# Kernel tuning notes

Measured on AMD Instinct MI355X. Metric: run time of the kernel, lower is better.

Reference implementation:

```python
import jax, jax.numpy as jnp
import numpy as np
import math

D_MODEL = 1024
N_HEADS = 16
D_HEAD = D_MODEL // N_HEADS


def setup_inputs() -> dict:
    key = jax.random.key(0)
    ks = jax.random.split(key, 5)
    scale = 1.0 / math.sqrt(D_MODEL)
    x = jax.random.normal(ks[0], (4, 2048, D_MODEL), dtype=jnp.float32)
    W_q = jax.random.uniform(ks[1], (D_MODEL, D_MODEL), jnp.float32, -scale, scale)
    W_k = jax.random.uniform(ks[2], (D_MODEL, D_MODEL), jnp.float32, -scale, scale)
    W_v = jax.random.uniform(ks[3], (D_MODEL, D_MODEL), jnp.float32, -scale, scale)
    W_o = jax.random.uniform(ks[4], (D_MODEL, D_MODEL), jnp.float32, -scale, scale)
    return {"x": x, "W_q": W_q, "W_k": W_k, "W_v": W_v, "W_o": W_o}


def reference(x, W_q, W_k, W_v, W_o):
    B, S, D = x.shape
    H, Dh = N_HEADS, D_HEAD
    # nn.Linear(bias=False): y = x @ W.T
    q = (x @ W_q.T).reshape(B, S, H, Dh).transpose(0, 2, 1, 3)  # [B,H,S,Dh]
    k = (x @ W_k.T).reshape(B, S, H, Dh).transpose(0, 2, 1, 3)
    v = (x @ W_v.T).reshape(B, S, H, Dh).transpose(0, 2, 1, 3)
    scores = jnp.einsum('bhqd,bhkd->bhqk', q, k) / math.sqrt(Dh)  # [B,H,S,S]
    causal = jnp.triu(jnp.ones((S, S), dtype=bool), k=1)
    scores = jnp.where(causal, jnp.float32(-1e9), scores)
    attn = jax.nn.softmax(scores, axis=-1)  # dropout = identity (eval)
    out = jnp.einsum('bhqk,bhkd->bhqd', attn, v)  # [B,H,S,Dh]
    out = out.transpose(0, 2, 1, 3).reshape(B, S, D)
    return out @ W_o.T
```

## Files before the change

kernel.cpp:

```cpp
#include <hip/hip_runtime.h>
#include <hip/hip_bf16.h>

typedef __attribute__((ext_vector_type(8))) short short8;
typedef __attribute__((ext_vector_type(4))) float f32x4;
typedef __attribute__((ext_vector_type(16))) float f32x16;
typedef __attribute__((ext_vector_type(4))) unsigned short u16x4;

#define S_LEN 2048
#define DH 64
#define NH 16
#define SCALE_LOG2 0.18033688011112042f
#define EXP2F(x) __builtin_amdgcn_exp2f(x)
#define GLOAD_LDS16(src, dst)                                             \
  __builtin_amdgcn_global_load_lds(                                       \
      (const __attribute__((address_space(1))) void*)(src),               \
      (__attribute__((address_space(3))) void*)(dst), 16, 0, 0)

__device__ __forceinline__ unsigned short f2bf(float f) {
  unsigned int u = __float_as_uint(f);
  u += 0x7fffu + ((u >> 16) & 1u);
  return (unsigned short)(u >> 16);
}

__device__ __forceinline__ unsigned int cvtpk(float a, float b) {
  unsigned int r;
  asm("v_cvt_pk_bf16_f32 %0, %1, %2" : "=v"(r) : "v"(a), "v"(b));
  return r;
}
__device__ __forceinline__ void plswap(unsigned int& a, unsigned int& b) {
  asm("v_permlane32_swap_b32 %0, %1" : "+v"(a), "+v"(b));
}

__global__ void convert_all(const float* __restrict__ x,
                            const float* __restrict__ w0,
                            const float* __restrict__ w1,
                            const float* __restrict__ w2,
                            const float* __restrict__ w3,
                            unsigned short* __restrict__ xb,
                            unsigned short* __restrict__ o0,
                            unsigned short* __restrict__ o1,
                            unsigned short* __restrict__ o2,
                            unsigned short* __restrict__ o3) {
  const int bid = blockIdx.x;
  const float* in;
  unsigned short* out;
  int i;
  if (bid < 8192) {
    in = x; out = xb;
    i = (bid * 256 + threadIdx.x) * 4;
  } else {
    const int seg = (bid - 8192) >> 10;
    in  = (seg == 0) ? w0 : (seg == 1) ? w1 : (seg == 2) ? w2 : w3;
    out = (seg == 0) ? o0 : (seg == 1) ? o1 : (seg == 2) ? o2 : o3;
    i = (((bid - 8192) & 1023) * 256 + threadIdx.x) * 4;
  }
  float4 v = *reinterpret_cast<const float4*>(in + i);
  u16x4 o;
  o.x = f2bf(v.x); o.y = f2bf(v.y); o.z = f2bf(v.z); o.w = f2bf(v.w);
  *reinterpret_cast<u16x4*>(out + i) = o;
}

template <int MODE>
__global__ __launch_bounds__(256) void gemm_bt(
    const unsigned short* __restrict__ A,
    const unsigned short* __restrict__ B,
    void* __restrict__ out, int M, int N, int K) {
  __shared__ __align__(16) unsigned short As[128 * 64];
  __shared__ __align__(16) unsigned short Bs[128 * 64];
  const int tid = threadIdx.x;
  const int l = tid & 63, w = tid >> 6;
  const int wr = w >> 1, wc = w & 1;
  const int g = l >> 4, c = l & 15;
  const int m0 = blockIdx.y * 128;
  const int n0 = blockIdx.x * 128;
  const int lrow = l >> 3, lcol = (l & 7) * 8;

  f32x4 acc[4][4] = {};

  for (int k0 = 0; k0 < K; k0 += 64) {
#pragma unroll
    for (int p = 0; p < 4; ++p) {
      int r0 = w * 32 + p * 8;
      GLOAD_LDS16(&A[(long)(m0 + r0 + lrow) * K + k0 + lcol], &As[r0 * 64]);
      GLOAD_LDS16(&B[(long)(n0 + r0 + lrow) * K + k0 + lcol], &Bs[r0 * 64]);
    }
    __syncthreads();
#pragma unroll
    for (int s = 0; s < 2; ++s) {
      short8 af[4], bf[4];
#pragma unroll
      for (int m = 0; m < 4; ++m)
        af[m] = *reinterpret_cast<const short8*>(
            &As[(wr * 64 + m * 16 + c) * 64 + s * 32 + g * 8]);
#pragma unroll
      for (int n = 0; n < 4; ++n)
        bf[n] = *reinterpret_cast<const short8*>(
            &Bs[(wc * 64 + n * 16 + c) * 64 + s * 32 + g * 8]);
#pragma unroll
      for (int m = 0; m < 4; ++m)
#pragma unroll
        for (int n = 0; n < 4; ++n)
          acc[m][n] = __builtin_amdgcn_mfma_f32_16x16x32_bf16(
              af[m], bf[n], acc[m][n], 0, 0, 0);
    }
    __syncthreads();
  }

#pragma unroll
  for (int m = 0; m < 4; ++m) {
#pragma unroll
    for (int n = 0; n < 4; ++n) {
#pragma unroll
      for (int r = 0; r < 4; ++r) {
        int row = m0 + wr * 64 + m * 16 + g * 4 + r;
        int col = n0 + wc * 64 + n * 16 + c;
        float v = acc[m][n][r];
        if (MODE == 3) {
          reinterpret_cast<float*>(out)[(long)row * N + col] = v;
        } else if (MODE == 2) {
          int b = row >> 11, s = row & 2047;
          int h = col >> 6, d = col & 63;
          reinterpret_cast<unsigned short*>(
              out)[((long)((b * NH + h) * DH + d)) * S_LEN + s] = f2bf(v);
        } else {
          if (MODE == 1) v *= SCALE_LOG2;
          int b = row >> 11, s = row & 2047;
          int h = col >> 6, d = col & 63;
          reinterpret_cast<unsigned short*>(
              out)[((long)((b * NH + h) * S_LEN + s)) * DH + d] = f2bf(v);
        }
      }
    }
  }
}

__device__ __forceinline__ int swz8c(int row, int chunk) {
  return row * 64 + ((chunk ^ (row & 7)) << 3);
}

__global__ __launch_bounds__(256) void attn_fwd(
    const unsigned short* __restrict__ Q, const unsigned short* __restrict__ Kg,
    const unsigned short* __restrict__ Vt, unsigned short* __restrict__ O) {
  __shared__ __align__(16) unsigned short Ks[2][64 * 64];
  __shared__ __align__(16) unsigned short Vs[2][64 * 64];

  const int tid = threadIdx.x;
  const int l = tid & 63, w = tid >> 6;
  const int ln = l & 31, hi = l >> 5, hi4 = hi * 4;
  const int bh = blockIdx.x;
  const int qb = 15 - blockIdx.y;
  const int b = bh >> 4, h = bh & 15;
  const long base = (long)bh * (S_LEN * DH);
  const int sr8 = l >> 3;
  const int scol = ((l & 7) ^ sr8) * 8;
  const int q0w = qb * 128 + w * 32;

  short8 qf[4];
  {
    const unsigned short* qp = Q + base + (long)(q0w + ln) * DH + hi * 8;
#pragma unroll
    for (int ks = 0; ks < 4; ++ks)
      qf[ks] = *reinterpret_cast<const short8*>(qp + ks * 16);
  }

  f32x16 o0 = {}, o1 = {};
  float m_r = -1e30f, l_r = 0.f;
  const int ntb = qb * 2 + 2;
  const int ntw = q0w / 64 + 1;

#pragma unroll
  for (int p = 0; p < 2; ++p) {
    int r0 = w * 16 + p * 8;
    GLOAD_LDS16(&Kg[base + (long)(r0 + sr8) * DH + scol], &Ks[0][r0 * 64]);
    GLOAD_LDS16(&Vt[base + (long)(r0 + sr8) * S_LEN + scol], &Vs[0][r0 * 64]);
  }
  __syncthreads();

  int cur = 0;
  for (int t = 0; t < ntb; ++t) {
    if (t + 1 < ntb) {
      const int kv1 = (t + 1) * 64;
#pragma unroll
      for (int p = 0; p < 2; ++p) {
        int r0 = w * 16 + p * 8;
        GLOAD_LDS16(&Kg[base + (long)(kv1 + r0 + sr8) * DH + scol],
                    &Ks[cur ^ 1][r0 * 64]);
        GLOAD_LDS16(&Vt[base + (long)(r0 + sr8) * S_LEN + kv1 + scol],
                    &Vs[cur ^ 1][r0 * 64]);
      }
    }
    if (t < ntw) {
      const unsigned short* ksb = Ks[cur];
      const unsigned short* vsb = Vs[cur];
      const int kv0 = t * 64;

      f32x16 s0 = {}, s1 = {};
      __builtin_amdgcn_s_setprio(1);
#pragma unroll
      for (int ks = 0; ks < 4; ++ks) {
        short8 ak0 =
            *reinterpret_cast<const short8*>(&ksb[swz8c(ln, ks * 2 + hi)]);
        short8 ak1 = *reinterpret_cast<const short8*>(
            &ksb[swz8c(32 + ln, ks * 2 + hi)]);
        s0 = __builtin_amdgcn_mfma_f32_32x32x16_bf16(ak0, qf[ks], s0, 0, 0, 0);
        s1 = __builtin_amdgcn_mfma_f32_32x32x16_bf16(ak1, qf[ks], s1, 0, 0, 0);
      }
      __builtin_amdgcn_s_setprio(0);

      if (t == ntw - 1) {
        const int qrel = (q0w - kv0) + ln;
#pragma unroll
        for (int r = 0; r < 16; ++r) {
          const int rowv = (r & 3) + 8 * (r >> 2) + hi4;
          if (rowv > qrel) s0[r] = -1e30f;
          if (rowv + 32 > qrel) s1[r] = -1e30f;
        }
      }

      float pm = -1e30f;
#pragma unroll
      for (int r = 0; r < 16; ++r) pm = fmaxf(pm, fmaxf(s0[r], s1[r]));
      pm = fmaxf(pm, __shfl_xor(pm, 32, 64));

      if (!__all(pm <= m_r + 8.0f)) {
        float mn = fmaxf(m_r, pm);
        float sc = EXP2F(m_r - mn);
        m_r = mn;
        l_r *= sc;
#pragma unroll
        for (int r = 0; r < 16; ++r) {
          float sv = __shfl(sc, (r & 3) + 8 * (r >> 2) + hi4, 64);
          o0[r] *= sv;
          o1[r] *= sv;
        }
      }

      float ps = 0.f;
#pragma unroll
      for (int r = 0; r < 16; ++r) {
        s0[r] = EXP2F(s0[r] - m_r);
        s1[r] = EXP2F(s1[r] - m_r);
        ps += s0[r] + s1[r];
      }
      ps += __shfl_xor(ps, 32, 64);
      l_r += ps;

      __builtin_amdgcn_s_setprio(1);
#pragma unroll
      for (int ks = 0; ks < 4; ++ks) {
        unsigned int wa, wb, wc2, wd;
        if (ks == 0) {
          wa = cvtpk(s0[0], s0[1]);   wc2 = cvtpk(s0[2], s0[3]);
          wb = cvtpk(s0[4], s0[5]);   wd  = cvtpk(s0[6], s0[7]);
        } else if (ks == 1) {
          wa = cvtpk(s0[8], s0[9]);   wc2 = cvtpk(s0[10], s0[11]);
          wb = cvtpk(s0[12], s0[13]); wd  = cvtpk(s0[14], s0[15]);
        } else if (ks == 2) {
          wa = cvtpk(s1[0], s1[1]);   wc2 = cvtpk(s1[2], s1[3]);
          wb = cvtpk(s1[4], s1[5]);   wd  = cvtpk(s1[6], s1[7]);
        } else {
          wa = cvtpk(s1[8], s1[9]);   wc2 = cvtpk(s1[10], s1[11]);
          wb = cvtpk(s1[12], s1[13]); wd  = cvtpk(s1[14], s1[15]);
        }
        plswap(wa, wb);
        plswap(wc2, wd);
        union { unsigned int u[4]; short8 s; } pa;
        pa.u[0] = wa; pa.u[1] = wc2; pa.u[2] = wb; pa.u[3] = wd;
        short8 v0 =
            *reinterpret_cast<const short8*>(&vsb[swz8c(ln, ks * 2 + hi)]);
        short8 v1 = *reinterpret_cast<const short8*>(
            &vsb[swz8c(32 + ln, ks * 2 + hi)]);
        o0 = __builtin_amdgcn_mfma_f32_32x32x16_bf16(pa.s, v0, o0, 0, 0, 0);
        o1 = __builtin_amdgcn_mfma_f32_32x32x16_bf16(pa.s, v1, o1, 0, 0, 0);
      }
      __builtin_amdgcn_s_setprio(0);
    }
    __syncthreads();
    cur ^= 1;
  }

  float inv = 1.0f / l_r;
#pragma unroll
  for (int r = 0; r < 16; ++r) {
    const int rowv = (r & 3) + 8 * (r >> 2) + hi4;
    float iv = __shfl(inv, rowv, 64);
    int q = q0w + rowv;
    long ob = ((long)(b * S_LEN + q)) * 1024 + h * 64 + ln;
    O[ob] = f2bf(o0[r] * iv);
    O[ob + 32] = f2bf(o1[r] * iv);
  }
}

extern "C" void kernel_launch(void* const* d_in, const int* in_sizes, int n_in,
                              void* d_out, int out_size, void* d_ws,
                              size_t ws_size, hipStream_t stream) {
  const float* x  = (const float*)d_in[0];
  const float* Wq = (const float*)d_in[1];
  const float* Wk = (const float*)d_in[2];
  const float* Wv = (const float*)d_in[3];
  const float* Wo = (const float*)d_in[4];
  float* out = (float*)d_out;
  char* ws = (char*)d_ws;

  unsigned short* xb  = (unsigned short*)(ws);
  unsigned short* Wqb = (unsigned short*)(ws + (16u << 20));
  unsigned short* Wkb = (unsigned short*)(ws + (18u << 20));
  unsigned short* Wvb = (unsigned short*)(ws + (20u << 20));
  unsigned short* Wob = (unsigned short*)(ws + (22u << 20));
  unsigned short* Vt  = (unsigned short*)(ws + (24u << 20));
  unsigned short* Ow  = (unsigned short*)(ws);
  unsigned short* Qw = (unsigned short*)d_out;
  unsigned short* Kw = (unsigned short*)d_out + (8u << 20);

  convert_all<<<12288, 256, 0, stream>>>(x, Wq, Wk, Wv, Wo, xb, Wqb, Wkb, Wvb,
                                         Wob);

  dim3 ggrid(8, 64);
  gemm_bt<1><<<ggrid, 256, 0, stream>>>(xb, Wqb, Qw, 8192, 1024, 1024);
  gemm_bt<0><<<ggrid, 256, 0, stream>>>(xb, Wkb, Kw, 8192, 1024, 1024);
  gemm_bt<2><<<ggrid, 256, 0, stream>>>(xb, Wvb, Vt, 8192, 1024, 1024);

  attn_fwd<<<dim3(64, 16), 256, 0, stream>>>(Qw, Kw, Vt, Ow);

  gemm_bt<3><<<ggrid, 256, 0, stream>>>(Ow, Wob, out, 8192, 1024, 1024);
}
```

Before: 194.9 us.

## Merge Q/K/V projection GEMMs into one launch with 8-wave blocks

The three separate Q, K and V projection GEMM launches become one launch, with blockIdx.z picking the weight matrix and the output layout. GEMM blocks grow from 4 to 8 waves, each wave now computing a 32x64 sub-tile instead of 64x64, which halves per-wave accumulator registers and adds waves for latency hiding. The output GEMM uses the same 8-wave configuration. The aim is to cut launch gaps and tail effects and to raise occupancy. The cost is less MFMA work per LDS fragment load for each wave and more intra-block synchronisation pressure.

Result: slower. 203.2 us (+4.3%).

```diff
diff --git a/kernel.cpp b/kernel.cpp
--- a/kernel.cpp
+++ b/kernel.cpp
@@ -61,10 +61,11 @@
 }
 
 template <int MODE>
-__global__ __launch_bounds__(256) void gemm_bt(
+__global__ __launch_bounds__(512) void gemm_bt(
     const unsigned short* __restrict__ A,
     const unsigned short* __restrict__ B,
-    void* __restrict__ out, int M, int N, int K) {
+    void* __restrict__ outQ, void* __restrict__ outK, void* __restrict__ outV,
+    int M, int N, int K) {
   __shared__ __align__(16) unsigned short As[128 * 64];
   __shared__ __align__(16) unsigned short Bs[128 * 64];
   const int tid = threadIdx.x;
@@ -73,31 +74,33 @@
   const int g = l >> 4, c = l & 15;
   const int m0 = blockIdx.y * 128;
   const int n0 = blockIdx.x * 128;
+  const int which = (MODE == 4) ? blockIdx.z : 0;
+  if (MODE == 4) B += (long)which << 20;
   const int lrow = l >> 3, lcol = (l & 7) * 8;
 
-  f32x4 acc[4][4] = {};
+  f32x4 acc[2][4] = {};
 
   for (int k0 = 0; k0 < K; k0 += 64) {
 #pragma unroll
-    for (int p = 0; p < 4; ++p) {
-      int r0 = w * 32 + p * 8;
+    for (int p = 0; p < 2; ++p) {
+      int r0 = p * 64 + w * 8;
       GLOAD_LDS16(&A[(long)(m0 + r0 + lrow) * K + k0 + lcol], &As[r0 * 64]);
       GLOAD_LDS16(&B[(long)(n0 + r0 + lrow) * K + k0 + lcol], &Bs[r0 * 64]);
     }
     __syncthreads();
 #pragma unroll
     for (int s = 0; s < 2; ++s) {
-      short8 af[4], bf[4];
-#pragma unroll
-      for (int m = 0; m < 4; ++m)
+      short8 af[2], bf[4];
+#pragma unroll
+      for (int m = 0; m < 2; ++m)
         af[m] = *reinterpret_cast<const short8*>(
-            &As[(wr * 64 + m * 16 + c) * 64 + s * 32 + g * 8]);
+            &As[(wr * 32 + m * 16 + c) * 64 + s * 32 + g * 8]);
 #pragma unroll
       for (int n = 0; n < 4; ++n)
         bf[n] = *reinterpret_cast<const short8*>(
             &Bs[(wc * 64 + n * 16 + c) * 64 + s * 32 + g * 8]);
 #pragma unroll
-      for (int m = 0; m < 4; ++m)
+      for (int m = 0; m < 2; ++m)
 #pragma unroll
         for (int n = 0; n < 4; ++n)
           acc[m][n] = __builtin_amdgcn_mfma_f32_16x16x32_bf16(
@@ -107,27 +110,30 @@
   }
 
 #pragma unroll
-  for (int m = 0; m < 4; ++m) {
+  for (int m = 0; m < 2; ++m) {
 #pragma unroll
     for (int n = 0; n < 4; ++n) {
 #pragma unroll
       for (int r = 0; r < 4; ++r) {
-        int row = m0 + wr * 64 + m * 16 + g * 4 + r;
+        int row = m0 + wr * 32 + m * 16 + g * 4 + r;
         int col = n0 + wc * 64 + n * 16 + c;
         float v = acc[m][n][r];
         if (MODE == 3) {
-          reinterpret_cast<float*>(out)[(long)row * N + col] = v;
-        } else if (MODE == 2) {
+          reinterpret_cast<float*>(outQ)[(long)row * N + col] = v;
+        } else {
           int b = row >> 11, s = row & 2047;
           int h = col >> 6, d = col & 63;
-          reinterpret_cast<unsigned short*>(
-              out)[((long)((b * NH + h) * DH + d)) * S_LEN + s] = f2bf(v);
-        } else {
-          if (MODE == 1) v *= SCALE_LOG2;
-          int b = row >> 11, s = row & 2047;
-          int h = col >> 6, d = col & 63;
-          reinterpret_cast<unsigned short*>(
-              out)[((long)((b * NH + h) * S_LEN + s)) * DH + d] = f2bf(v);
+          if (which == 0) {
+            reinterpret_cast<unsigned short*>(
+                outQ)[((long)((b * NH + h) * S_LEN + s)) * DH + d] =
+                f2bf(v * SCALE_LOG2);
+          } else if (which == 1) {
+            reinterpret_cast<unsigned short*>(
+                outK)[((long)((b * NH + h) * S_LEN + s)) * DH + d] = f2bf(v);
+          } else {
+            reinterpret_cast<unsigned short*>(
+                outV)[((long)((b * NH + h) * DH + d)) * S_LEN + s] = f2bf(v);
+          }
         }
       }
     }
@@ -315,12 +321,11 @@
   convert_all<<<12288, 256, 0, stream>>>(x, Wq, Wk, Wv, Wo, xb, Wqb, Wkb, Wvb,
                                          Wob);
 
-  dim3 ggrid(8, 64);
-  gemm_bt<1><<<ggrid, 256, 0, stream>>>(xb, Wqb, Qw, 8192, 1024, 1024);
-  gemm_bt<0><<<ggrid, 256, 0, stream>>>(xb, Wkb, Kw, 8192, 1024, 1024);
-  gemm_bt<2><<<ggrid, 256, 0, stream>>>(xb, Wvb, Vt, 8192, 1024, 1024);
+  gemm_bt<4><<<dim3(8, 64, 3), 512, 0, stream>>>(xb, Wqb, Qw, Kw, Vt,
+                                                 8192, 1024, 1024);
 
   attn_fwd<<<dim3(64, 16), 256, 0, stream>>>(Qw, Kw, Vt, Ow);
 
-  gemm_bt<3><<<ggrid, 256, 0, stream>>>(Ow, Wob, out, 8192, 1024, 1024);
-}
+  gemm_bt<3><<<dim3(8, 64), 512, 0, stream>>>(Ow, Wob, out, nullptr, nullptr,
+                                              8192, 1024, 1024);
+}
```

## Double-buffer GEMM LDS tiles with XOR swizzle and MFMA priority

Applied to the files above, without the earlier changes.

The projection GEMM now uses two LDS buffers so the global-to-LDS load of the next K tile is issued while the current tile is consumed by MFMAs, removing one barrier per iteration. LDS writes and reads use an XOR chunk swizzle to avoid bank conflicts on fragment loads, and s_setprio raises wave priority around the MFMA block. LDS use doubles to 64KB per block, which may reduce occupancy.

New measurement: 179.3 us. 8.0% less time.

```diff
diff --git a/kernel.cpp b/kernel.cpp
--- a/kernel.cpp
+++ b/kernel.cpp
@@ -29,6 +29,10 @@
 }
 __device__ __forceinline__ void plswap(unsigned int& a, unsigned int& b) {
   asm("v_permlane32_swap_b32 %0, %1" : "+v"(a), "+v"(b));
+}
+
+__device__ __forceinline__ int swz8c(int row, int chunk) {
+  return row * 64 + ((chunk ^ (row & 7)) << 3);
 }
 
 __global__ void convert_all(const float* __restrict__ x,
@@ -65,46 +69,60 @@
     const unsigned short* __restrict__ A,
     const unsigned short* __restrict__ B,
     void* __restrict__ out, int M, int N, int K) {
-  __shared__ __align__(16) unsigned short As[128 * 64];
-  __shared__ __align__(16) unsigned short Bs[128 * 64];
+  __shared__ __align__(16) unsigned short As[2][128 * 64];
+  __shared__ __align__(16) unsigned short Bs[2][128 * 64];
   const int tid = threadIdx.x;
   const int l = tid & 63, w = tid >> 6;
   const int wr = w >> 1, wc = w & 1;
   const int g = l >> 4, c = l & 15;
   const int m0 = blockIdx.y * 128;
   const int n0 = blockIdx.x * 128;
-  const int lrow = l >> 3, lcol = (l & 7) * 8;
+  const int sr8 = l >> 3;
+  const int scol = ((l & 7) ^ sr8) * 8;
 
   f32x4 acc[4][4] = {};
 
+#define GSTAGE(buf, k0)                                                     \
+  do {                                                                      \
+    _Pragma("unroll") for (int p = 0; p < 4; ++p) {                         \
+      int r0 = w * 32 + p * 8;                                              \
+      GLOAD_LDS16(&A[(long)(m0 + r0 + sr8) * K + (k0) + scol],              \
+                  &As[buf][r0 * 64]);                                       \
+      GLOAD_LDS16(&B[(long)(n0 + r0 + sr8) * K + (k0) + scol],              \
+                  &Bs[buf][r0 * 64]);                                       \
+    }                                                                       \
+  } while (0)
+
+  GSTAGE(0, 0);
+  __syncthreads();
+
+  int cur = 0;
   for (int k0 = 0; k0 < K; k0 += 64) {
-#pragma unroll
-    for (int p = 0; p < 4; ++p) {
-      int r0 = w * 32 + p * 8;
-      GLOAD_LDS16(&A[(long)(m0 + r0 + lrow) * K + k0 + lcol], &As[r0 * 64]);
-      GLOAD_LDS16(&B[(long)(n0 + r0 + lrow) * K + k0 + lcol], &Bs[r0 * 64]);
-    }
-    __syncthreads();
+    if (k0 + 64 < K) GSTAGE(cur ^ 1, k0 + 64);
 #pragma unroll
     for (int s = 0; s < 2; ++s) {
       short8 af[4], bf[4];
 #pragma unroll
       for (int m = 0; m < 4; ++m)
         af[m] = *reinterpret_cast<const short8*>(
-            &As[(wr * 64 + m * 16 + c) * 64 + s * 32 + g * 8]);
+            &As[cur][swz8c(wr * 64 + m * 16 + c, s * 4 + g)]);
 #pragma unroll
       for (int n = 0; n < 4; ++n)
         bf[n] = *reinterpret_cast<const short8*>(
-            &Bs[(wc * 64 + n * 16 + c) * 64 + s * 32 + g * 8]);
+            &Bs[cur][swz8c(wc * 64 + n * 16 + c, s * 4 + g)]);
+      __builtin_amdgcn_s_setprio(1);
 #pragma unroll
       for (int m = 0; m < 4; ++m)
 #pragma unroll
         for (int n = 0; n < 4; ++n)
           acc[m][n] = __builtin_amdgcn_mfma_f32_16x16x32_bf16(
               af[m], bf[n], acc[m][n], 0, 0, 0);
+      __builtin_amdgcn_s_setprio(0);
     }
     __syncthreads();
-  }
+    cur ^= 1;
+  }
+#undef GSTAGE
 
 #pragma unroll
   for (int m = 0; m < 4; ++m) {
@@ -132,10 +150,6 @@
       }
     }
   }
-}
-
-__device__ __forceinline__ int swz8c(int row, int chunk) {
-  return row * 64 + ((chunk ^ (row & 7)) << 3);
 }
 
 __global__ __launch_bounds__(256) void attn_fwd(
```
